# Optimization experiments

Hardware: AMD Instinct MI355X
Metric: run time of the kernel (lower is better)

The kernel has to match this reference:

```python
import jax, jax.numpy as jnp
import numpy as np

B, N, DIM, H, DH = 2, 2048, 1024, 16, 64
SCALE = 8.0
LN_EPS = 1e-5
L2_EPS = 1e-12


def setup_inputs() -> dict:
    key = jax.random.key(0)
    ks = jax.random.split(key, 6)
    s = 0.02  # keep projections at sane magnitude
    return {
        "x": jax.random.normal(ks[0], (B, N, DIM), dtype=jnp.float32),
        "g": jnp.ones((DIM,), dtype=jnp.float32),
        "b": jnp.zeros((DIM,), dtype=jnp.float32),
        "c_attn_w": jax.random.normal(ks[1], (DIM, 3 * DIM), dtype=jnp.float32) * s,
        "c_attn_b": jax.random.normal(ks[2], (3 * DIM,), dtype=jnp.float32) * s,
        "c_proj_w": jax.random.normal(ks[3], (DIM, DIM), dtype=jnp.float32) * s,
        "c_proj_b": jax.random.normal(ks[4], (DIM,), dtype=jnp.float32) * s,
        "to_out_w": jax.random.normal(ks[5], (DIM, DIM), dtype=jnp.float32) * s,
    }


def _l2norm(t):
    # F.normalize(t, dim=-1): t / max(||t||, eps)
    n = jnp.sqrt(jnp.sum(t * t, axis=-1, keepdims=True))
    return t / jnp.maximum(n, L2_EPS)


def reference(x, g, b, c_attn_w, c_attn_b, c_proj_w, c_proj_b, to_out_w):
    # LayerNorm
    mu = jnp.mean(x, axis=-1, keepdims=True)
    var = jnp.mean(jnp.square(x - mu), axis=-1, keepdims=True)
    y = (x - mu) * jax.lax.rsqrt(var + LN_EPS) * g + b  # [B,N,DIM]

    # GPT2 Conv1D c_attn: y @ W + b, split into q/k/v
    qkv = y @ c_attn_w + c_attn_b  # [B,N,3*DIM]
    q, k, v = jnp.split(qkv, 3, axis=-1)

    def split_heads(t):
        return t.reshape(B, N, H, DH).transpose(0, 2, 1, 3)  # [B,H,N,DH]

    q, k, v = split_heads(q), split_heads(k), split_heads(v)

    # cosine-sim attention: L2-normalize q,k, scaled dot product, causal softmax
    qn, kn = _l2norm(q), _l2norm(k)
    sim = jnp.einsum("bhid,bhjd->bhij", qn, kn) * SCALE  # [B,H,N,N]
    mask_value = -jnp.finfo(sim.dtype).max
    causal = jnp.triu(jnp.ones((N, N), dtype=bool), k=1)
    sim = jnp.where(causal, mask_value, sim)
    attn = jax.nn.softmax(sim, axis=-1)
    o = jnp.einsum("bhij,bhjd->bhid", attn, v)  # [B,H,N,DH]

    o = o.transpose(0, 2, 1, 3).reshape(B, N, DIM)
    o = o @ c_proj_w + c_proj_b          # Conv1D c_proj
    out = o @ to_out_w.T                  # Linear to_out (no bias)
    return out
```

## Files before the change

### kernel.cpp

```cpp
#include <hip/hip_runtime.h>
#include <cstdint>
#include <cstddef>

#define Bb 2
#define Nn 2048
#define DIMM 1024
#define Hh 16
#define DHh 64
#define BH (Bb*Hh)
#define MROWS (Bb*Nn)

typedef __bf16 bf16x8 __attribute__((ext_vector_type(8)));
typedef float f32x4 __attribute__((ext_vector_type(4)));
typedef short s16x4 __attribute__((ext_vector_type(4)));

__device__ __forceinline__ unsigned short f2bf(float f) {
  unsigned u = __float_as_uint(f);
  u += 0x7FFFu + ((u >> 16) & 1u);
  return (unsigned short)(u >> 16);
}
__device__ __forceinline__ unsigned short f2bf_fast(float f) {
  return (unsigned short)((__float_as_uint(f) + 0x8000u) >> 16);
}
__device__ __forceinline__ float bf2f(unsigned short s) {
  return __uint_as_float(((unsigned)s) << 16);
}

#define GLDS16(g, l) __builtin_amdgcn_global_load_lds( \
    (const __attribute__((address_space(1))) void*)(g), \
    (__attribute__((address_space(3))) void*)(l), 16, 0, 0)

__global__ __launch_bounds__(256) void prep_kernel(
    const float* __restrict__ x, const float* __restrict__ g,
    const float* __restrict__ b,
    const float* __restrict__ c_attn_w, const float* __restrict__ c_proj_w,
    const float* __restrict__ to_out_w, const float* __restrict__ c_proj_b,
    unsigned short* __restrict__ y,
    unsigned short* __restrict__ wqkv, unsigned short* __restrict__ wpbf,
    unsigned short* __restrict__ wout, float* __restrict__ bc) {
  int bid = blockIdx.x;
  int t = threadIdx.x;
  if (bid < 4096) {
    int row = bid;
    const float4* xr = (const float4*)(x + (size_t)row * DIMM);
    float4 v = xr[t];
    float s  = v.x + v.y + v.z + v.w;
    float ss = v.x*v.x + v.y*v.y + v.z*v.z + v.w*v.w;
    #pragma unroll
    for (int o = 1; o < 64; o <<= 1) { s += __shfl_xor(s, o); ss += __shfl_xor(ss, o); }
    __shared__ float red[8];
    int wv = t >> 6;
    if ((t & 63) == 0) { red[wv] = s; red[wv + 4] = ss; }
    __syncthreads();
    s  = red[0] + red[1] + red[2] + red[3];
    ss = red[4] + red[5] + red[6] + red[7];
    float mu  = s * (1.0f / DIMM);
    float var = ss * (1.0f / DIMM) - mu * mu;
    float rs  = rsqrtf(var + 1e-5f);
    float4 gv = ((const float4*)g)[t];
    float4 bv = ((const float4*)b)[t];
    ushort4 o4;
    o4.x = f2bf((v.x - mu) * rs * gv.x + bv.x);
    o4.y = f2bf((v.y - mu) * rs * gv.y + bv.y);
    o4.z = f2bf((v.z - mu) * rs * gv.z + bv.z);
    o4.w = f2bf((v.w - mu) * rs * gv.w + bv.w);
    ((ushort4*)y)[(size_t)row * 256 + t] = o4;
  } else if (bid < 7168) {
    __shared__ float tile[32][33];
    int bb = bid - 4096;
    int bx = bb % 96, by = bb / 96;
    int tx = t & 31, ty = t >> 5;
    int x2 = bx * 32 + tx;
    int y0 = by * 32;
    #pragma unroll
    for (int j = 0; j < 32; j += 8)
      tile[ty + j][tx] = c_attn_w[(size_t)(y0 + ty + j) * 3072 + x2];
    __syncthreads();
    int ox  = by * 32 + tx;
    int oy0 = bx * 32;
    #pragma unroll
    for (int j = 0; j < 32; j += 8)
      wqkv[(size_t)(oy0 + ty + j) * 1024 + ox] = f2bf(tile[tx][ty + j]);
  } else if (bid < 9216) {
    bool iswp = bid < 8192;
    int bb = bid - (iswp ? 7168 : 8192);
    const float* in = iswp ? c_proj_w : to_out_w;
    unsigned short* out = iswp ? wpbf : wout;
    int i = (bb * 256 + t) * 4;
    float4 v = *(const float4*)(in + i);
    ushort4 o;
    o.x = f2bf(v.x); o.y = f2bf(v.y); o.z = f2bf(v.z); o.w = f2bf(v.w);
    *(ushort4*)(out + i) = o;
  } else {
    int n = (bid - 9216) * 4 + (t >> 6);
    int lane = t & 63;
    const float4* w = (const float4*)(to_out_w + (size_t)n * DIMM);
    const float4* b4 = (const float4*)c_proj_b;
    float s = 0.0f;
    #pragma unroll
    for (int k = 0; k < 4; k++) {
      float4 wv = w[lane + k * 64], bv = b4[lane + k * 64];
      s += wv.x * bv.x + wv.y * bv.y + wv.z * bv.z + wv.w * bv.w;
    }
    #pragma unroll
    for (int o = 1; o < 64; o <<= 1) s += __shfl_xor(s, o);
    if (lane == 0) bc[n] = s;
  }
}

template <int EPI>
__device__ __forceinline__ void gemm_body(
    const unsigned short* __restrict__ A, const unsigned short* __restrict__ Bt,
    const float* __restrict__ bias,
    unsigned short* __restrict__ obf, float* __restrict__ of32,
    unsigned short* __restrict__ q_std, unsigned short* __restrict__ k_std,
    unsigned short* __restrict__ vt_out,
    int M, int N, int K, int bn, int bm,
    unsigned short* smem) {
  int t = threadIdx.x;
  int lane = t & 63, wv = t >> 6;
  int wm = (wv >> 1) * 32, wn = (wv & 1) * 64;
  int l16 = lane & 15, quad = lane >> 4;

  const unsigned short* Ab = A + (size_t)(bm * 128) * K;
  const unsigned short* Bb2 = Bt + (size_t)(bn * 128) * K;
  int srow = t >> 3;
  int gch = (t & 7) ^ (srow & 7);

  f32x4 acc[2][4] = {};
  const int KT = K >> 6;

  auto stage = [&](int kt_, int b_) {
    unsigned short* dA = smem + b_ * 16384;
    unsigned short* dB = dA + 8192;
    const unsigned short* gA = Ab  + (size_t)srow * K + kt_ * 64 + gch * 8;
    const unsigned short* gB = Bb2 + (size_t)srow * K + kt_ * 64 + gch * 8;
    #pragma unroll
    for (int i = 0; i < 2; i++) {
      GLDS16(gA + (size_t)(64 * i) * K, dA + (size_t)(t + 512 * i) * 8);
      GLDS16(gB + (size_t)(64 * i) * K, dB + (size_t)(t + 512 * i) * 8);
    }
  };

  stage(0, 0);
  if (KT > 1) stage(1, 1);

  for (int kt2 = 0; kt2 < KT; ++kt2) {
    if (kt2 < KT - 1) asm volatile("s_waitcnt vmcnt(4)" ::: "memory");
    else              asm volatile("s_waitcnt vmcnt(0)" ::: "memory");
    __builtin_amdgcn_s_barrier();
    __builtin_amdgcn_sched_barrier(0);
    const unsigned short* sA = smem + (kt2 & 1) * 16384;
    const unsigned short* sB = sA + 8192;
    #pragma unroll
    for (int kk = 0; kk < 2; kk++) {
      int slot = (kk * 4 + quad) ^ (l16 & 7);
      bf16x8 af[2], bfr[4];
      #pragma unroll
      for (int i = 0; i < 2; i++)
        af[i] = *(const bf16x8*)(sA + (size_t)(wm + i * 16 + l16) * 64 + slot * 8);
      #pragma unroll
      for (int j = 0; j < 4; j++)
        bfr[j] = *(const bf16x8*)(sB + (size_t)(wn + j * 16 + l16) * 64 + slot * 8);
      __builtin_amdgcn_s_setprio(1);
      #pragma unroll
      for (int i = 0; i < 2; i++)
        #pragma unroll
        for (int j = 0; j < 4; j++)
          acc[i][j] = __builtin_amdgcn_mfma_f32_16x16x32_bf16(af[i], bfr[j], acc[i][j], 0, 0, 0);
      __builtin_amdgcn_s_setprio(0);
    }
    __builtin_amdgcn_sched_barrier(0);
    __builtin_amdgcn_s_barrier();
    __builtin_amdgcn_sched_barrier(0);
    if (kt2 + 2 < KT) stage(kt2 + 2, kt2 & 1);
  }

  float bvals[4];
  #pragma unroll
  for (int j = 0; j < 4; j++)
    bvals[j] = (EPI == 3) ? 0.0f : bias[bn * 128 + wn + j * 16 + l16];

  if (EPI == 0) {
    int which = bn >> 3;
    if (which < 2) {
      #pragma unroll
      for (int i = 0; i < 2; i++) {
        #pragma unroll
        for (int r = 0; r < 4; r++) {
          int m = bm * 128 + wm + i * 16 + quad * 4 + r;
          float vals[4];
          float ss = 0.0f;
          #pragma unroll
          for (int j = 0; j < 4; j++) {
            vals[j] = acc[i][j][r] + bvals[j];
            ss += vals[j] * vals[j];
          }
          ss += __shfl_xor(ss, 1); ss += __shfl_xor(ss, 2);
          ss += __shfl_xor(ss, 4); ss += __shfl_xor(ss, 8);
          float scale = ((which == 0) ? 8.0f : 1.0f) / fmaxf(sqrtf(ss), 1e-12f);
          int bi = m >> 11, ns = m & 2047;
          unsigned short* dst = (which == 0) ? q_std : k_std;
          #pragma unroll
          for (int j = 0; j < 4; j++) {
            int n = bn * 128 + wn + j * 16 + l16;
            int nn2 = n & 1023;
            int h = nn2 >> 6, d = nn2 & 63;
            dst[((size_t)((bi * Hh + h) * Nn + ns)) * DHh + d] = f2bf(vals[j] * scale);
          }
        }
      }
    } else {
      __syncthreads();
      #pragma unroll
      for (int i = 0; i < 2; i++) {
        int mchunk = (wm + i * 16) / 4 + quad;
        #pragma unroll
        for (int j = 0; j < 4; j++) {
          int n_local = wn + j * 16 + l16;
          int sw = mchunk ^ (n_local & 31);
          ushort4 pack;
          pack.x = f2bf(acc[i][j][0] + bvals[j]);
          pack.y = f2bf(acc[i][j][1] + bvals[j]);
          pack.z = f2bf(acc[i][j][2] + bvals[j]);
          pack.w = f2bf(acc[i][j][3] + bvals[j]);
          *(ushort4*)(smem + (size_t)n_local * 128 + sw * 4) = pack;
        }
      }
      __syncthreads();
      int drow = t >> 2, mq = t & 3;
      int h = (bn - 16) * 2 + (drow >> 6);
      int d = drow & 63;
      int bi = bm >> 4;
      int ns0 = (bm * 128) & 2047;
      unsigned short* dst = vt_out + ((size_t)(bi * Hh + h) * DHh + d) * Nn + ns0 + mq * 32;
      #pragma unroll
      for (int cc = 0; cc < 8; cc++) {
        int c0 = mq * 8 + cc;
        int s0 = c0 ^ (drow & 31);
        *(ushort4*)(dst + cc * 4) = *(const ushort4*)(smem + (size_t)drow * 128 + s0 * 4);
      }
    }
  } else {
    #pragma unroll
    for (int i = 0; i < 2; i++) {
      #pragma unroll
      for (int j = 0; j < 4; j++) {
        int n = bn * 128 + wn + j * 16 + l16;
        #pragma unroll
        for (int r = 0; r < 4; r++) {
          int m = bm * 128 + wm + i * 16 + quad * 4 + r;
          float val = acc[i][j][r] + bvals[j];
          if (EPI == 2) of32[(size_t)m * N + n] = val;
          else          obf[(size_t)m * N + n] = f2bf(val);
        }
      }
    }
  }
}

__global__ __launch_bounds__(512, 4) void gemm_qkv_wcomb(
    const unsigned short* __restrict__ y, const unsigned short* __restrict__ wqkv,
    const float* __restrict__ c_attn_b,
    unsigned short* __restrict__ q_std, unsigned short* __restrict__ k_std,
    unsigned short* __restrict__ vt_out,
    const unsigned short* __restrict__ wout, const unsigned short* __restrict__ wpbf,
    unsigned short* __restrict__ wcomb) {
  __shared__ unsigned short smem[32768];
  int bn = blockIdx.x, bm = blockIdx.y;
  if (bn < 24) {
    gemm_body<0>(y, wqkv, c_attn_b, nullptr, nullptr, q_std, k_std, vt_out,
                 MROWS, 3 * DIMM, DIMM, bn, bm, smem);
  } else {
    int idx = (bn - 24) * 32 + bm;
    gemm_body<3>(wout, wpbf, nullptr, wcomb, nullptr, nullptr, nullptr, nullptr,
                 DIMM, DIMM, DIMM, idx & 7, idx >> 3, smem);
  }
}

__global__ __launch_bounds__(512, 4) void gemm_final(
    const unsigned short* __restrict__ A, const unsigned short* __restrict__ Bt,
    const float* __restrict__ bias, float* __restrict__ of32) {
  __shared__ unsigned short smem[32768];
  gemm_body<2>(A, Bt, bias, nullptr, of32, nullptr, nullptr, nullptr,
               MROWS, DIMM, DIMM, blockIdx.x, blockIdx.y, smem);
}

__global__ __launch_bounds__(512, 4) void attn_kernel(
    const unsigned short* __restrict__ qn, const unsigned short* __restrict__ kn,
    const unsigned short* __restrict__ vt, unsigned short* __restrict__ o_flat) {
  __shared__ float smemf[16384];
  int t = threadIdx.x, lane = t & 63, wv = t >> 6;
  int half = wv >> 2, strip = wv & 3;
  int l16 = lane & 15, quad = lane >> 4;
  int id = blockIdx.x;
  int qb = (id < 256) ? (15 - (id >> 5)) : ((id - 256) >> 5);
  int bh = id & 31;
  int m0 = qb * 128 + strip * 32;
  const unsigned short* qbase = qn + (size_t)bh * Nn * DHh;
  const unsigned short* kbase = kn + (size_t)bh * Nn * DHh;
  const unsigned short* vbase = vt + (size_t)bh * DHh * Nn;

  bf16x8 aq[2][2];
  #pragma unroll
  for (int i2 = 0; i2 < 2; i2++)
    #pragma unroll
    for (int kk = 0; kk < 2; kk++)
      aq[i2][kk] = *(const bf16x8*)(qbase + (size_t)(m0 + i2 * 16 + l16) * DHh + kk * 32 + quad * 8);

  f32x4 accOT[4][2] = {};
  float den[2] = {};

  int tl = t & 255;
  int srow = tl >> 3;
  int gch = (tl & 7) ^ (srow & 7);
  int nh = qb + 1;
  int kt0 = half * nh;

  auto stageT = [&](int kt_, int b_) {
    int jj = (kt0 + kt_) * 64;
    unsigned short* K_ = (unsigned short*)((char*)smemf + half * 32768 + b_ * 16384);
    unsigned short* V_ = K_ + 4096;
    GLDS16(kbase + (size_t)(jj + srow)      * DHh + gch * 8, K_ + (size_t)tl * 8);
    GLDS16(kbase + (size_t)(jj + srow + 32) * DHh + gch * 8, K_ + (size_t)(tl + 256) * 8);
    GLDS16(vbase + (size_t)srow        * Nn + jj + gch * 8, V_ + (size_t)tl * 8);
    GLDS16(vbase + (size_t)(srow + 32) * Nn + jj + gch * 8, V_ + (size_t)(tl + 256) * 8);
  };

  stageT(0, 0);
  if (nh > 1) stageT(1, 1);

  for (int kt = 0; kt < nh; kt++) {
    if (kt < nh - 1) asm volatile("s_waitcnt vmcnt(4)" ::: "memory");
    else             asm volatile("s_waitcnt vmcnt(0)" ::: "memory");
    __builtin_amdgcn_s_barrier();
    __builtin_amdgcn_sched_barrier(0);
    int j0 = (kt0 + kt) * 64;
    unsigned short* myK = (unsigned short*)((char*)smemf + half * 32768 + (kt & 1) * 16384);
    unsigned short* myV = myK + 4096;

    if (j0 <= m0 + 31) {
      f32x4 sc[4][2] = {};
      #pragma unroll
      for (int kk = 0; kk < 2; kk++) {
        int slot = (kk * 4 + quad) ^ (l16 & 7);
        #pragma unroll
        for (int jt = 0; jt < 4; jt++) {
          bf16x8 ak = *(const bf16x8*)(myK + (size_t)(jt * 16 + l16) * 64 + slot * 8);
          #pragma unroll
          for (int i2 = 0; i2 < 2; i2++)
            sc[jt][i2] = __builtin_amdgcn_mfma_f32_16x16x32_bf16(ak, aq[i2][kk], sc[jt][i2], 0, 0, 0);
        }
      }

      bool fullTile = (j0 + 63) <= m0;
      s16x4 pf[4][2];
      #pragma unroll
      for (int jt = 0; jt < 4; jt++) {
        #pragma unroll
        for (int i2 = 0; i2 < 2; i2++) {
          int m = m0 + i2 * 16 + l16;
          #pragma unroll
          for (int r = 0; r < 4; r++) {
            int j = j0 + jt * 16 + quad * 4 + r;
            float p;
            if (fullTile) p = __expf(sc[jt][i2][r] - 8.0f);
            else          p = (j <= m) ? __expf(sc[jt][i2][r] - 8.0f) : 0.0f;
            den[i2] += p;
            pf[jt][i2][r] = (short)f2bf_fast(p);
          }
        }
      }

      #pragma unroll
      for (int jt = 0; jt < 4; jt++) {
        #pragma unroll
        for (int dt = 0; dt < 4; dt++) {
          int row = dt * 16 + l16;
          int ch = (jt * 2 + (quad >> 1)) ^ (l16 & 7);
          s16x4 av = *(const s16x4*)(myV + (size_t)row * 64 + ch * 8 + (quad & 1) * 4);
          #pragma unroll
          for (int i2 = 0; i2 < 2; i2++)
            accOT[dt][i2] = __builtin_amdgcn_mfma_f32_16x16x16bf16_1k(av, pf[jt][i2], accOT[dt][i2], 0, 0, 0);
        }
      }
    }

    __builtin_amdgcn_sched_barrier(0);
    __builtin_amdgcn_s_barrier();
    __builtin_amdgcn_sched_barrier(0);
    if (kt + 2 < nh) stageT(kt + 2, kt & 1);
  }

  #pragma unroll
  for (int i2 = 0; i2 < 2; i2++) {
    float d = den[i2];
    d += __shfl_xor(d, 16); d += __shfl_xor(d, 32);
    den[i2] = d;
  }

  __syncthreads();
  float* scr = smemf + strip * 2176;
  if (half == 1) {
    #pragma unroll
    for (int dt = 0; dt < 4; dt++)
      #pragma unroll
      for (int i2 = 0; i2 < 2; i2++)
        *(f32x4*)(scr + ((size_t)(dt * 2 + i2) * 64 + lane) * 4) = accOT[dt][i2];
    scr[2048 + lane] = den[0];
    scr[2048 + 64 + lane] = den[1];
  }
  __syncthreads();
  if (half == 0) {
    float dinv[2];
    dinv[0] = 1.0f / (den[0] + scr[2048 + lane]);
    dinv[1] = 1.0f / (den[1] + scr[2048 + 64 + lane]);
    int bi = bh >> 4, h = bh & 15;
    #pragma unroll
    for (int i2 = 0; i2 < 2; i2++) {
      #pragma unroll
      for (int dt = 0; dt < 4; dt++) {
        f32x4 o = accOT[dt][i2] + *(const f32x4*)(scr + ((size_t)(dt * 2 + i2) * 64 + lane) * 4);
        ushort4 o4;
        o4.x = f2bf(o[0] * dinv[i2]);
        o4.y = f2bf(o[1] * dinv[i2]);
        o4.z = f2bf(o[2] * dinv[i2]);
        o4.w = f2bf(o[3] * dinv[i2]);
        int ns = m0 + i2 * 16 + l16;
        int d0 = dt * 16 + quad * 4;
        *(ushort4*)(o_flat + ((size_t)(bi * Nn + ns)) * DIMM + h * DHh + d0) = o4;
      }
    }
  }
}

extern "C" void kernel_launch(void* const* d_in, const int* in_sizes, int n_in,
                              void* d_out, int out_size, void* d_ws, size_t ws_size,
                              hipStream_t stream) {
  const float* x        = (const float*)d_in[0];
  const float* g        = (const float*)d_in[1];
  const float* b        = (const float*)d_in[2];
  const float* c_attn_w = (const float*)d_in[3];
  const float* c_attn_b = (const float*)d_in[4];
  const float* c_proj_w = (const float*)d_in[5];
  const float* c_proj_b = (const float*)d_in[6];
  const float* to_out_w = (const float*)d_in[7];
  float* out = (float*)d_out;

  char* p = (char*)d_ws;
  unsigned short* y     = (unsigned short*)(p + ((size_t)0  << 20));
  unsigned short* qbuf  = (unsigned short*)(p + ((size_t)8  << 20));
  unsigned short* kbuf  = (unsigned short*)(p + ((size_t)16 << 20));
  unsigned short* vtb   = (unsigned short*)(p + ((size_t)24 << 20));
  unsigned short* wpbf  = (unsigned short*)(p + ((size_t)32 << 20));
  unsigned short* wout  = (unsigned short*)(p + ((size_t)34 << 20));
  unsigned short* wqkv  = (unsigned short*)(p + ((size_t)40 << 20));
  unsigned short* wcomb = (unsigned short*)(p + ((size_t)46 << 20));
  float*          bc    = (float*)        (p + ((size_t)48 << 20));

  prep_kernel<<<9472, 256, 0, stream>>>(x, g, b, c_attn_w, c_proj_w, to_out_w,
                                        c_proj_b, y, wqkv, wpbf, wout, bc);
  gemm_qkv_wcomb<<<dim3(26, MROWS / 128), 512, 0, stream>>>(
      y, wqkv, c_attn_b, qbuf, kbuf, vtb, wout, wpbf, wcomb);
  attn_kernel<<<512, 512, 0, stream>>>(qbuf, kbuf, vtb, y);
  gemm_final<<<dim3(DIMM / 128, MROWS / 128), 512, 0, stream>>>(y, wcomb, bc, out);
}
```

Measured before the change: 199.7 us.

## Restructure attention into 64-row query tiles without split-KV merge

The attention kernel now uses 256-thread blocks, each owning a 64-row query tile (16 rows per wave) and walking all causal key tiles itself. This removes the two-half split over keys and the LDS-based merge of partial accumulators and denominators. Blocks are interleaved so long and short causal tiles pair up, and head indices are spread across the grid. The trade-off is that K/V tiles loaded into LDS are now reused by 64 query rows instead of 128, so global/LDS traffic per FLOP roughly doubles.

After: 210.0 us. 5.2% more time.

```diff
diff --git a/kernel.cpp b/kernel.cpp
--- a/kernel.cpp
+++ b/kernel.cpp
@@ -286,45 +286,41 @@
                MROWS, DIMM, DIMM, blockIdx.x, blockIdx.y, smem);
 }
 
-__global__ __launch_bounds__(512, 4) void attn_kernel(
+__global__ __launch_bounds__(256, 4) void attn_kernel(
     const unsigned short* __restrict__ qn, const unsigned short* __restrict__ kn,
     const unsigned short* __restrict__ vt, unsigned short* __restrict__ o_flat) {
-  __shared__ float smemf[16384];
-  int t = threadIdx.x, lane = t & 63, wv = t >> 6;
-  int half = wv >> 2, strip = wv & 3;
+  __shared__ float smemf[8192];
+  int t = threadIdx.x, lane = t & 63, strip = t >> 6;
   int l16 = lane & 15, quad = lane >> 4;
   int id = blockIdx.x;
-  int qb = (id < 256) ? (15 - (id >> 5)) : ((id - 256) >> 5);
-  int bh = id & 31;
-  int m0 = qb * 128 + strip * 32;
+  int bh = ((id & 7) << 2) | (id >> 8);
+  int pid = (id >> 3) & 31;
+  int qb2 = (pid & 1) ? (pid >> 1) : (31 - (pid >> 1));
+  int m0 = qb2 * 64 + strip * 16;
   const unsigned short* qbase = qn + (size_t)bh * Nn * DHh;
   const unsigned short* kbase = kn + (size_t)bh * Nn * DHh;
   const unsigned short* vbase = vt + (size_t)bh * DHh * Nn;
 
-  bf16x8 aq[2][2];
+  bf16x8 aq[2];
   #pragma unroll
-  for (int i2 = 0; i2 < 2; i2++)
-    #pragma unroll
-    for (int kk = 0; kk < 2; kk++)
-      aq[i2][kk] = *(const bf16x8*)(qbase + (size_t)(m0 + i2 * 16 + l16) * DHh + kk * 32 + quad * 8);
-
-  f32x4 accOT[4][2] = {};
-  float den[2] = {};
-
-  int tl = t & 255;
-  int srow = tl >> 3;
-  int gch = (tl & 7) ^ (srow & 7);
-  int nh = qb + 1;
-  int kt0 = half * nh;
+  for (int kk = 0; kk < 2; kk++)
+    aq[kk] = *(const bf16x8*)(qbase + (size_t)(m0 + l16) * DHh + kk * 32 + quad * 8);
+
+  f32x4 accOT[4] = {};
+  float den = 0.0f;
+
+  int srow = t >> 3;
+  int gch = (t & 7) ^ (srow & 7);
+  int nh = qb2 + 1;
 
   auto stageT = [&](int kt_, int b_) {
-    int jj = (kt0 + kt_) * 64;
-    unsigned short* K_ = (unsigned short*)((char*)smemf + half * 32768 + b_ * 16384);
+    int jj = kt_ * 64;
+    unsigned short* K_ = (unsigned short*)((char*)smemf + b_ * 16384);
     unsigned short* V_ = K_ + 4096;
-    GLDS16(kbase + (size_t)(jj + srow)      * DHh + gch * 8, K_ + (size_t)tl * 8);
-    GLDS16(kbase + (size_t)(jj + srow + 32) * DHh + gch * 8, K_ + (size_t)(tl + 256) * 8);
-    GLDS16(vbase + (size_t)srow        * Nn + jj + gch * 8, V_ + (size_t)tl * 8);
-    GLDS16(vbase + (size_t)(srow + 32) * Nn + jj + gch * 8, V_ + (size_t)(tl + 256) * 8);
+    GLDS16(kbase + (size_t)(jj + srow)      * DHh + gch * 8, K_ + (size_t)t * 8);
+    GLDS16(kbase + (size_t)(jj + srow + 32) * DHh + gch * 8, K_ + (size_t)(t + 256) * 8);
+    GLDS16(vbase + (size_t)srow        * Nn + jj + gch * 8, V_ + (size_t)t * 8);
+    GLDS16(vbase + (size_t)(srow + 32) * Nn + jj + gch * 8, V_ + (size_t)(t + 256) * 8);
   };
 
   stageT(0, 0);
@@ -335,40 +331,35 @@
     else             asm volatile("s_waitcnt vmcnt(0)" ::: "memory");
     __builtin_amdgcn_s_barrier();
     __builtin_amdgcn_sched_barrier(0);
-    int j0 = (kt0 + kt) * 64;
-    unsigned short* myK = (unsigned short*)((char*)smemf + half * 32768 + (kt & 1) * 16384);
+    int j0 = kt * 64;
+    unsigned short* myK = (unsigned short*)((char*)smemf + (kt & 1) * 16384);
     unsigned short* myV = myK + 4096;
 
-    if (j0 <= m0 + 31) {
-      f32x4 sc[4][2] = {};
+    if (j0 <= m0 + 15) {
+      f32x4 sc[4] = {};
       #pragma unroll
       for (int kk = 0; kk < 2; kk++) {
         int slot = (kk * 4 + quad) ^ (l16 & 7);
         #pragma unroll
         for (int jt = 0; jt < 4; jt++) {
           bf16x8 ak = *(const bf16x8*)(myK + (size_t)(jt * 16 + l16) * 64 + slot * 8);
-          #pragma unroll
-          for (int i2 = 0; i2 < 2; i2++)
-            sc[jt][i2] = __builtin_amdgcn_mfma_f32_16x16x32_bf16(ak, aq[i2][kk], sc[jt][i2], 0, 0, 0);
+          sc[jt] = __builtin_amdgcn_mfma_f32_16x16x32_bf16(ak, aq[kk], sc[jt], 0, 0, 0);
         }
       }
 
       bool fullTile = (j0 + 63) <= m0;
-      s16x4 pf[4][2];
+      int m = m0 + l16;
+      s16x4 pf[4];
       #pragma unroll
       for (int jt = 0; jt < 4; jt++) {
         #pragma unroll
-        for (int i2 = 0; i2 < 2; i2++) {
-          int m = m0 + i2 * 16 + l16;
-          #pragma unroll
-          for (int r = 0; r < 4; r++) {
-            int j = j0 + jt * 16 + quad * 4 + r;
-            float p;
-            if (fullTile) p = __expf(sc[jt][i2][r] - 8.0f);
-            else          p = (j <= m) ? __expf(sc[jt][i2][r] - 8.0f) : 0.0f;
-            den[i2] += p;
-            pf[jt][i2][r] = (short)f2bf_fast(p);
-          }
+        for (int r = 0; r < 4; r++) {
+          int j = j0 + jt * 16 + quad * 4 + r;
+          float p;
+          if (fullTile) p = __expf(sc[jt][r] - 8.0f);
+          else          p = (j <= m) ? __expf(sc[jt][r] - 8.0f) : 0.0f;
+          den += p;
+          pf[jt][r] = (short)f2bf_fast(p);
         }
       }
 
@@ -379,9 +370,7 @@
           int row = dt * 16 + l16;
           int ch = (jt * 2 + (quad >> 1)) ^ (l16 & 7);
           s16x4 av = *(const s16x4*)(myV + (size_t)row * 64 + ch * 8 + (quad & 1) * 4);
-          #pragma unroll
-          for (int i2 = 0; i2 < 2; i2++)
-            accOT[dt][i2] = __builtin_amdgcn_mfma_f32_16x16x16bf16_1k(av, pf[jt][i2], accOT[dt][i2], 0, 0, 0);
+          accOT[dt] = __builtin_amdgcn_mfma_f32_16x16x16bf16_1k(av, pf[jt], accOT[dt], 0, 0, 0);
         }
       }
     }
@@ -392,45 +381,22 @@
     if (kt + 2 < nh) stageT(kt + 2, kt & 1);
   }
 
+  den += __shfl_xor(den, 16);
+  den += __shfl_xor(den, 32);
+  float dinv = 1.0f / den;
+
+  int bi = bh >> 4, h = bh & 15;
+  int ns = m0 + l16;
   #pragma unroll
-  for (int i2 = 0; i2 < 2; i2++) {
-    float d = den[i2];
-    d += __shfl_xor(d, 16); d += __shfl_xor(d, 32);
-    den[i2] = d;
-  }
-
-  __syncthreads();
-  float* scr = smemf + strip * 2176;
-  if (half == 1) {
-    #pragma unroll
-    for (int dt = 0; dt < 4; dt++)
-      #pragma unroll
-      for (int i2 = 0; i2 < 2; i2++)
-        *(f32x4*)(scr + ((size_t)(dt * 2 + i2) * 64 + lane) * 4) = accOT[dt][i2];
-    scr[2048 + lane] = den[0];
-    scr[2048 + 64 + lane] = den[1];
-  }
-  __syncthreads();
-  if (half == 0) {
-    float dinv[2];
-    dinv[0] = 1.0f / (den[0] + scr[2048 + lane]);
-    dinv[1] = 1.0f / (den[1] + scr[2048 + 64 + lane]);
-    int bi = bh >> 4, h = bh & 15;
-    #pragma unroll
-    for (int i2 = 0; i2 < 2; i2++) {
-      #pragma unroll
-      for (int dt = 0; dt < 4; dt++) {
-        f32x4 o = accOT[dt][i2] + *(const f32x4*)(scr + ((size_t)(dt * 2 + i2) * 64 + lane) * 4);
-        ushort4 o4;
-        o4.x = f2bf(o[0] * dinv[i2]);
-        o4.y = f2bf(o[1] * dinv[i2]);
-        o4.z = f2bf(o[2] * dinv[i2]);
-        o4.w = f2bf(o[3] * dinv[i2]);
-        int ns = m0 + i2 * 16 + l16;
-        int d0 = dt * 16 + quad * 4;
-        *(ushort4*)(o_flat + ((size_t)(bi * Nn + ns)) * DIMM + h * DHh + d0) = o4;
-      }
-    }
+  for (int dt = 0; dt < 4; dt++) {
+    f32x4 o = accOT[dt];
+    ushort4 o4;
+    o4.x = f2bf(o[0] * dinv);
+    o4.y = f2bf(o[1] * dinv);
+    o4.z = f2bf(o[2] * dinv);
+    o4.w = f2bf(o[3] * dinv);
+    int d0 = dt * 16 + quad * 4;
+    *(ushort4*)(o_flat + ((size_t)(bi * Nn + ns)) * DIMM + h * DHh + d0) = o4;
   }
 }
 
@@ -462,6 +428,6 @@
                                         c_proj_b, y, wqkv, wpbf, wout, bc);
   gemm_qkv_wcomb<<<dim3(26, MROWS / 128), 512, 0, stream>>>(
       y, wqkv, c_attn_b, qbuf, kbuf, vtb, wout, wpbf, wcomb);
-  attn_kernel<<<512, 512, 0, stream>>>(qbuf, kbuf, vtb, y);
+  attn_kernel<<<1024, 256, 0, stream>>>(qbuf, kbuf, vtb, y);
   gemm_final<<<dim3(DIMM / 128, MROWS / 128), 512, 0, stream>>>(y, wcomb, bc, out);
 }
```

## Use 128-wide single-buffered KV tiles and exp2-based softmax in attention

Applied to the files above, without the earlier changes.

The attention loop now stages 128-key tiles of K and V into a single LDS buffer per half instead of double-buffered 64-key tiles, so each iteration waits for its own loads with no prefetch overlap. The Q scale is folded to 8/ln2 so the softmax can use the raw v_exp_f32 (exp2) instruction directly. Bounds masking is extended to handle the split point between the two halves. This halves the number of loop iterations and barriers and cuts exp cost, but it gives up the overlap of global loads with compute.

After: 198.3 us. About the same (-0.7%).

```diff
diff --git a/kernel.cpp b/kernel.cpp
--- a/kernel.cpp
+++ b/kernel.cpp
@@ -198,7 +198,7 @@
           }
           ss += __shfl_xor(ss, 1); ss += __shfl_xor(ss, 2);
           ss += __shfl_xor(ss, 4); ss += __shfl_xor(ss, 8);
-          float scale = ((which == 0) ? 8.0f : 1.0f) / fmaxf(sqrtf(ss), 1e-12f);
+          float scale = ((which == 0) ? 11.5415603f : 1.0f) / fmaxf(sqrtf(ss), 1e-12f);
           int bi = m >> 11, ns = m & 2047;
           unsigned short* dst = (which == 0) ? q_std : k_std;
           #pragma unroll
@@ -312,84 +312,87 @@
   float den[2] = {};
 
   int tl = t & 255;
-  int srow = tl >> 3;
-  int gch = (tl & 7) ^ (srow & 7);
-  int nh = qb + 1;
-  int kt0 = half * nh;
-
-  auto stageT = [&](int kt_, int b_) {
-    int jj = (kt0 + kt_) * 64;
-    unsigned short* K_ = (unsigned short*)((char*)smemf + half * 32768 + b_ * 16384);
-    unsigned short* V_ = K_ + 4096;
-    GLDS16(kbase + (size_t)(jj + srow)      * DHh + gch * 8, K_ + (size_t)tl * 8);
-    GLDS16(kbase + (size_t)(jj + srow + 32) * DHh + gch * 8, K_ + (size_t)(tl + 256) * 8);
-    GLDS16(vbase + (size_t)srow        * Nn + jj + gch * 8, V_ + (size_t)tl * 8);
-    GLDS16(vbase + (size_t)(srow + 32) * Nn + jj + gch * 8, V_ + (size_t)(tl + 256) * 8);
+  int nh2 = (qb + 2) >> 1;
+  int jstart = half * ((qb + 1) * 64);
+  int jlim = half ? Nn : (qb + 1) * 64;
+
+  unsigned short* K_ = (unsigned short*)((char*)smemf + half * 32768);
+  unsigned short* V_ = K_ + 8192;
+
+  int krow = tl >> 3;
+  int kg   = (tl & 7) ^ (krow & 7);
+  int vrow = tl >> 4;
+  int vg   = (tl & 15) ^ vrow;
+
+  auto stageT = [&](int kt_) {
+    int j0 = jstart + kt_ * 128;
+    #pragma unroll
+    for (int i = 0; i < 4; i++)
+      GLDS16(kbase + (size_t)(j0 + krow + 32 * i) * DHh + kg * 8, K_ + (size_t)(tl + 256 * i) * 8);
+    #pragma unroll
+    for (int i = 0; i < 4; i++)
+      GLDS16(vbase + (size_t)(vrow + 16 * i) * Nn + j0 + vg * 8, V_ + (size_t)(tl + 256 * i) * 8);
   };
 
-  stageT(0, 0);
-  if (nh > 1) stageT(1, 1);
-
-  for (int kt = 0; kt < nh; kt++) {
-    if (kt < nh - 1) asm volatile("s_waitcnt vmcnt(4)" ::: "memory");
-    else             asm volatile("s_waitcnt vmcnt(0)" ::: "memory");
+  for (int kt = 0; kt < nh2; kt++) {
+    int j0 = jstart + kt * 128;
+    __builtin_amdgcn_s_barrier();
+    stageT(kt);
+    asm volatile("s_waitcnt vmcnt(0)" ::: "memory");
     __builtin_amdgcn_s_barrier();
     __builtin_amdgcn_sched_barrier(0);
-    int j0 = (kt0 + kt) * 64;
-    unsigned short* myK = (unsigned short*)((char*)smemf + half * 32768 + (kt & 1) * 16384);
-    unsigned short* myV = myK + 4096;
 
     if (j0 <= m0 + 31) {
-      f32x4 sc[4][2] = {};
-      #pragma unroll
-      for (int kk = 0; kk < 2; kk++) {
-        int slot = (kk * 4 + quad) ^ (l16 & 7);
+      s16x4 pf[8][2];
+      #pragma unroll
+      for (int pass = 0; pass < 2; pass++) {
+        f32x4 sc[4][2] = {};
+        #pragma unroll
+        for (int kk = 0; kk < 2; kk++) {
+          int slot = (kk * 4 + quad) ^ (l16 & 7);
+          #pragma unroll
+          for (int jt = 0; jt < 4; jt++) {
+            int row = (pass * 4 + jt) * 16 + l16;
+            bf16x8 ak = *(const bf16x8*)(K_ + (size_t)row * 64 + slot * 8);
+            #pragma unroll
+            for (int i2 = 0; i2 < 2; i2++)
+              sc[jt][i2] = __builtin_amdgcn_mfma_f32_16x16x32_bf16(ak, aq[i2][kk], sc[jt][i2], 0, 0, 0);
+          }
+        }
+        int jp = j0 + pass * 64;
+        bool full = (jp + 63 <= m0) && (jp + 64 <= jlim);
         #pragma unroll
         for (int jt = 0; jt < 4; jt++) {
-          bf16x8 ak = *(const bf16x8*)(myK + (size_t)(jt * 16 + l16) * 64 + slot * 8);
           #pragma unroll
-          for (int i2 = 0; i2 < 2; i2++)
-            sc[jt][i2] = __builtin_amdgcn_mfma_f32_16x16x32_bf16(ak, aq[i2][kk], sc[jt][i2], 0, 0, 0);
-        }
-      }
-
-      bool fullTile = (j0 + 63) <= m0;
-      s16x4 pf[4][2];
-      #pragma unroll
-      for (int jt = 0; jt < 4; jt++) {
-        #pragma unroll
-        for (int i2 = 0; i2 < 2; i2++) {
-          int m = m0 + i2 * 16 + l16;
-          #pragma unroll
-          for (int r = 0; r < 4; r++) {
-            int j = j0 + jt * 16 + quad * 4 + r;
-            float p;
-            if (fullTile) p = __expf(sc[jt][i2][r] - 8.0f);
-            else          p = (j <= m) ? __expf(sc[jt][i2][r] - 8.0f) : 0.0f;
-            den[i2] += p;
-            pf[jt][i2][r] = (short)f2bf_fast(p);
+          for (int i2 = 0; i2 < 2; i2++) {
+            int m = m0 + i2 * 16 + l16;
+            #pragma unroll
+            for (int r = 0; r < 4; r++) {
+              int j = jp + jt * 16 + quad * 4 + r;
+              float e = sc[jt][i2][r] - 11.5415603f;
+              float p;
+              asm("v_exp_f32 %0, %1" : "=v"(p) : "v"(e));
+              if (!full && (j > m || j >= jlim)) p = 0.0f;
+              den[i2] += p;
+              pf[pass * 4 + jt][i2][r] = (short)f2bf_fast(p);
+            }
           }
         }
       }
-
-      #pragma unroll
-      for (int jt = 0; jt < 4; jt++) {
+      #pragma unroll
+      for (int jt = 0; jt < 8; jt++) {
+        int cj = 2 * jt + (quad >> 1);
         #pragma unroll
         for (int dt = 0; dt < 4; dt++) {
           int row = dt * 16 + l16;
-          int ch = (jt * 2 + (quad >> 1)) ^ (l16 & 7);
-          s16x4 av = *(const s16x4*)(myV + (size_t)row * 64 + ch * 8 + (quad & 1) * 4);
+          int cs = cj ^ l16;
+          s16x4 av = *(const s16x4*)(V_ + (size_t)row * 128 + cs * 8 + (quad & 1) * 4);
           #pragma unroll
           for (int i2 = 0; i2 < 2; i2++)
             accOT[dt][i2] = __builtin_amdgcn_mfma_f32_16x16x16bf16_1k(av, pf[jt][i2], accOT[dt][i2], 0, 0, 0);
         }
       }
     }
-
-    __builtin_amdgcn_sched_barrier(0);
-    __builtin_amdgcn_s_barrier();
-    __builtin_amdgcn_sched_barrier(0);
-    if (kt + 2 < nh) stageT(kt + 2, kt & 1);
   }
 
   #pragma unroll
```
